# Performance work log

Measured on AMD Instinct MI355X. Metric: run time of the kernel, lower is better.

The kernel has to match this reference:

```python
import jax, jax.numpy as jnp
import numpy as np

DY, DO, DI = 16, 256, 256
BS = 4096
EPS = 1e-6


def setup_inputs() -> dict:
    key = jax.random.key(0)
    k1, k2, k3, k4, k5 = jax.random.split(key, 5)
    k = 1.0 / float(np.sqrt(DY * DI))
    return {
        "x": jax.random.normal(k1, (DY * DI, BS), dtype=jnp.float32),
        "rms_params": jnp.ones((DY * DI,), dtype=jnp.float32)
        + 0.01 * jax.random.normal(k2, (DY * DI,), dtype=jnp.float32),
        "w_upper": jax.random.uniform(k3, (DY, DO, DI), minval=-k, maxval=k, dtype=jnp.float32),
        "w_lower": jax.random.uniform(k4, (DY, DO, DI), minval=-k, maxval=k, dtype=jnp.float32),
        "bias": jax.random.uniform(k5, (DY * DO,), minval=-k, maxval=k, dtype=jnp.float32),
    }


def reference(x, rms_params, w_upper, w_lower, bias):
    # x: (dy*di, bs) features-first layout, matching the torch op.
    dy, do, di = w_upper.shape
    bs = x.shape[1]
    # Per-column RMS factor (fc in the original op is shape (bs,)).
    fc = jax.lax.rsqrt(jnp.mean(x * x, axis=0) + EPS)  # (bs,)
    xn = x * rms_params[:, None] * fc[None, :]          # fused norm+scale
    xb = xn.reshape(dy, di, bs)
    # Dyadic structured matmul: upper acts on block d, lower on its paired
    # (reversed) block dy-1-d.
    up = jnp.einsum("doi,dib->dob", w_upper, xb)
    lo = jnp.einsum("doi,dib->dob", w_lower, xb[::-1])
    y = jax.nn.relu(up + lo + bias.reshape(dy, do, 1))
    return y.reshape(dy * do, bs)
```

## Files before the change

### kernel.cpp

```cpp
#include <hip/hip_runtime.h>

#define DYN 16
#define DON 256
#define DIN 256
#define BSN 4096
#define NF 4096
#define KTOT 512

typedef unsigned short u16;
typedef __attribute__((ext_vector_type(8))) short bf16x8;
typedef __attribute__((ext_vector_type(4))) float f32x4;
typedef __attribute__((ext_vector_type(4))) unsigned short u16x4;

static __device__ __forceinline__ u16 f2bf(float f) {
  unsigned u = __builtin_bit_cast(unsigned, f);
  u += 0x7fffu + ((u >> 16) & 1u);
  return (u16)(u >> 16);
}
static __device__ __forceinline__ float bf2f(u16 h) {
  unsigned u = ((unsigned)h) << 16;
  return __builtin_bit_cast(float, u);
}

__global__ __launch_bounds__(256) void k_pre(
    const float* __restrict__ x, const float* __restrict__ wu,
    const float* __restrict__ wl, const float* __restrict__ rms,
    u16* __restrict__ aprep, u16* __restrict__ xbf,
    float* __restrict__ partial) {
  __shared__ u16 tile[128 * 132];
  const int t = threadIdx.x;
  if (blockIdx.x < 1024) {
    int e = blockIdx.x * 256 + t;
    int row = e >> 6;
    int k0 = (e & 63) << 3;
    int d = row >> 8;
    const float* src;
    const float* rp;
    if (k0 < 256) {
      src = wu + (size_t)row * 256 + k0;
      rp  = rms + d * 256 + k0;
    } else {
      src = wl + (size_t)row * 256 + (k0 - 256);
      rp  = rms + (DYN - 1 - d) * 256 + (k0 - 256);
    }
    float4 s0 = *reinterpret_cast<const float4*>(src);
    float4 s1 = *reinterpret_cast<const float4*>(src + 4);
    float4 r0 = *reinterpret_cast<const float4*>(rp);
    float4 r1 = *reinterpret_cast<const float4*>(rp + 4);
    bf16x8 o;
    o[0] = (short)f2bf(s0.x * r0.x); o[1] = (short)f2bf(s0.y * r0.y);
    o[2] = (short)f2bf(s0.z * r0.z); o[3] = (short)f2bf(s0.w * r0.w);
    o[4] = (short)f2bf(s1.x * r1.x); o[5] = (short)f2bf(s1.y * r1.y);
    o[6] = (short)f2bf(s1.z * r1.z); o[7] = (short)f2bf(s1.w * r1.w);
    *reinterpret_cast<bf16x8*>(aprep + (size_t)row * KTOT + k0) = o;
    return;
  }
  const int bid = blockIdx.x - 1024;
  const int bt = bid & 31, ft = bid >> 5;
  const float* xb = x + (size_t)ft * 128 * BSN + bt * 128;
  const int frow = t >> 5, b4 = (t & 31) * 4;
  #pragma unroll
  for (int p = 0; p < 16; ++p) {
    int f = p * 8 + frow;
    float4 v = *reinterpret_cast<const float4*>(xb + (size_t)f * BSN + b4);
    u16x4 h;
    h[0] = f2bf(v.x); h[1] = f2bf(v.y); h[2] = f2bf(v.z); h[3] = f2bf(v.w);
    *reinterpret_cast<u16x4*>(&tile[f * 132 + b4]) = h;
  }
  __syncthreads();
  const int chunk = t & 15;
  const int bg = t >> 4;
  #pragma unroll
  for (int p = 0; p < 8; ++p) {
    int b = bg + p * 16;
    float s = 0.f;
    bf16x8 w;
    #pragma unroll
    for (int jj = 0; jj < 8; ++jj) {
      int j = (jj + chunk) & 7;
      u16 v = tile[(chunk * 8 + j) * 132 + b];
      float xv = bf2f(v);
      s += xv * xv;
      w[j] = (short)v;
    }
    *reinterpret_cast<bf16x8*>(
        xbf + (size_t)(bt * 128 + b) * NF + ft * 128 + chunk * 8) = w;
    #pragma unroll
    for (int m = 1; m < 16; m <<= 1) s += __shfl_xor(s, m, 64);
    if (chunk == 0) partial[ft * BSN + bt * 128 + b] = s;
  }
}

__global__ __launch_bounds__(512, 4) void k_gemm(
    const u16* __restrict__ aprep, const u16* __restrict__ xbf,
    const float* __restrict__ partial, const float* __restrict__ bias,
    float* __restrict__ out) {
  extern __shared__ char smem[];
  float* fcl = (float*)(smem + 73728);
  const int bid = blockIdx.x;
  const int dp = bid & 7;
  const int s = bid >> 3;
  const int d = (s & 1) ? (15 - dp) : dp;
  const int fh = (s >> 1) & 1;
  const int bt = s >> 2;
  const int b0 = bt * 256;
  const int fr0 = d * 256 + fh * 128;
  const int t = threadIdx.x;
  const int wave = t >> 6, lane = t & 63;
  const int lhi = lane >> 4, llo = lane & 15;
  const int wm = wave >> 2, wn = wave & 3;
  const int kmask = ((llo >> 1) & 7) << 4;

  auto stage = [&](int slot, int kt) {
    const int fbase = (kt < 8) ? (d * 256 + kt * 32)
                               : ((15 - d) * 256 + (kt - 8) * 32);
    #pragma unroll
    for (int j = 0; j < 2; ++j) {
      int c = j * 512 + t;
      int cl = c ^ ((c >> 3) & 7);
      int r = cl >> 2, kc = cl & 3;
      const u16* g = xbf + (size_t)(b0 + r) * NF + fbase + kc * 8;
      unsigned lbase = (unsigned)(slot * 24576 + (j * 512 + wave * 64) * 16);
      __builtin_amdgcn_global_load_lds(
          (const __attribute__((address_space(1))) unsigned int*)g,
          (__attribute__((address_space(3))) unsigned int*)(smem + lbase),
          16, 0, 0);
    }
    {
      int c = t;
      int cl = c ^ ((c >> 3) & 7);
      int r = cl >> 2, kc = cl & 3;
      const u16* g = aprep + (size_t)(fr0 + r) * KTOT + kt * 32 + kc * 8;
      unsigned lbase = (unsigned)(slot * 24576 + 16384 + (wave * 64) * 16);
      __builtin_amdgcn_global_load_lds(
          (const __attribute__((address_space(1))) unsigned int*)g,
          (__attribute__((address_space(3))) unsigned int*)(smem + lbase),
          16, 0, 0);
    }
  };

  if (t < 256) {
    float fs = 0.f;
    #pragma unroll
    for (int i = 0; i < 32; ++i) fs += partial[i * BSN + b0 + t];
    fcl[t] = rsqrtf(fs * (1.0f / 4096.0f) + 1e-6f);
  }

  f32x4 acc[8][2];
  #pragma unroll
  for (int m = 0; m < 8; ++m)
    #pragma unroll
    for (int n = 0; n < 2; ++n)
      acc[m][n] = f32x4{0.f, 0.f, 0.f, 0.f};

  stage(0, 0);
  stage(1, 1);
  asm volatile("s_waitcnt vmcnt(3)\n\ts_barrier" ::: "memory");

  for (int kt = 0; kt < 16; ++kt) {
    const int slot = kt % 3;
    const char* sA = (const char*)smem + slot * 24576;
    const char* sB = sA + 16384;
    if (kt < 14) stage((kt + 2) % 3, kt + 2);

    bf16x8 bq[2], af[4];
    #pragma unroll
    for (int n = 0; n < 2; ++n) {
      int row = wn * 32 + n * 16 + llo;
      bq[n] = *reinterpret_cast<const bf16x8*>(
          sB + ((row * 64 + lhi * 16) ^ kmask));
    }
    #pragma unroll
    for (int m = 0; m < 4; ++m) {
      int row = wm * 128 + m * 16 + llo;
      af[m] = *reinterpret_cast<const bf16x8*>(
          sA + ((row * 64 + lhi * 16) ^ kmask));
    }
    __builtin_amdgcn_s_setprio(1);
    #pragma unroll
    for (int m = 0; m < 4; ++m)
      #pragma unroll
      for (int n = 0; n < 2; ++n)
        acc[m][n] = __builtin_amdgcn_mfma_f32_16x16x32_bf16(
            af[m], bq[n], acc[m][n], 0, 0, 0);
    __builtin_amdgcn_s_setprio(0);
    #pragma unroll
    for (int m = 0; m < 4; ++m) {
      int row = wm * 128 + 64 + m * 16 + llo;
      af[m] = *reinterpret_cast<const bf16x8*>(
          sA + ((row * 64 + lhi * 16) ^ kmask));
    }
    __builtin_amdgcn_s_setprio(1);
    #pragma unroll
    for (int m = 0; m < 4; ++m)
      #pragma unroll
      for (int n = 0; n < 2; ++n)
        acc[4 + m][n] = __builtin_amdgcn_mfma_f32_16x16x32_bf16(
            af[m], bq[n], acc[4 + m][n], 0, 0, 0);
    __builtin_amdgcn_s_setprio(0);

    if (kt < 14) {
      asm volatile("s_waitcnt vmcnt(3)\n\ts_barrier" ::: "memory");
    } else if (kt == 14) {
      asm volatile("s_waitcnt vmcnt(0)\n\ts_barrier" ::: "memory");
    }
  }

  #pragma unroll
  for (int m = 0; m < 8; ++m) {
    int lb = wm * 128 + m * 16 + lhi * 4;
    float4 fq = *reinterpret_cast<const float4*>(&fcl[lb]);
    #pragma unroll
    for (int n = 0; n < 2; ++n) {
      int fo = fr0 + wn * 32 + n * 16 + llo;
      float bv = bias[fo];
      float4 v;
      v.x = fmaxf(acc[m][n][0] * fq.x + bv, 0.f);
      v.y = fmaxf(acc[m][n][1] * fq.y + bv, 0.f);
      v.z = fmaxf(acc[m][n][2] * fq.z + bv, 0.f);
      v.w = fmaxf(acc[m][n][3] * fq.w + bv, 0.f);
      *reinterpret_cast<float4*>(out + (size_t)fo * BSN + b0 + lb) = v;
    }
  }
}

extern "C" void kernel_launch(void* const* d_in, const int* in_sizes, int n_in,
                              void* d_out, int out_size, void* d_ws, size_t ws_size,
                              hipStream_t stream) {
  (void)in_sizes; (void)n_in; (void)out_size; (void)ws_size;
  const float* x    = (const float*)d_in[0];
  const float* rms  = (const float*)d_in[1];
  const float* wu   = (const float*)d_in[2];
  const float* wl   = (const float*)d_in[3];
  const float* bias = (const float*)d_in[4];
  float* out = (float*)d_out;

  char* ws = (char*)d_ws;
  u16* xbf      = (u16*)ws;
  u16* aprep    = (u16*)(ws + 33554432);
  float* partial = (float*)(ws + 37748736);

  k_pre<<<2048, 256, 0, stream>>>(x, wu, wl, rms, aprep, xbf, partial);
  k_gemm<<<512, 512, 74752, stream>>>(aprep, xbf, partial, bias, out);
}
```

Measured before the change: 57.51 us.

## Retile GEMM to 128x256 blocks with 4 waves and swizzle pre-pass LDS tile

The GEMM block tile changes from 256 batch x 128 features with 8 waves to 128 batch x 256 features with 4 waves. Each wave now holds a 64x128 accumulator tile, which gives more MFMA work per LDS fragment load, and the weight tile is staged in four async loads instead of one. Separately, the pre-pass LDS transpose tile uses an XOR swizzle on the column index in place of the rotated read order, to cut bank conflicts. Risks are higher register pressure from 128 accumulator floats per thread and fewer waves per block, which reduces the ability to hide latency.

```diff
diff --git a/kernel.cpp b/kernel.cpp
--- a/kernel.cpp
+++ b/kernel.cpp
@@ -65,7 +65,7 @@
     float4 v = *reinterpret_cast<const float4*>(xb + (size_t)f * BSN + b4);
     u16x4 h;
     h[0] = f2bf(v.x); h[1] = f2bf(v.y); h[2] = f2bf(v.z); h[3] = f2bf(v.w);
-    *reinterpret_cast<u16x4*>(&tile[f * 132 + b4]) = h;
+    *reinterpret_cast<u16x4*>(&tile[f * 132 + (b4 ^ ((f >> 3) << 2))]) = h;
   }
   __syncthreads();
   const int chunk = t & 15;
@@ -76,9 +76,9 @@
     float s = 0.f;
     bf16x8 w;
     #pragma unroll
-    for (int jj = 0; jj < 8; ++jj) {
-      int j = (jj + chunk) & 7;
-      u16 v = tile[(chunk * 8 + j) * 132 + b];
+    for (int j = 0; j < 8; ++j) {
+      int r = chunk * 8 + j;
+      u16 v = tile[r * 132 + (b ^ ((r >> 3) << 2))];
       float xv = bf2f(v);
       s += xv * xv;
       w[j] = (short)v;
@@ -91,7 +91,7 @@
   }
 }
 
-__global__ __launch_bounds__(512, 4) void k_gemm(
+__global__ __launch_bounds__(256, 2) void k_gemm(
     const u16* __restrict__ aprep, const u16* __restrict__ xbf,
     const float* __restrict__ partial, const float* __restrict__ bias,
     float* __restrict__ out) {
@@ -101,37 +101,45 @@
   const int dp = bid & 7;
   const int s = bid >> 3;
   const int d = (s & 1) ? (15 - dp) : dp;
-  const int fh = (s >> 1) & 1;
-  const int bt = s >> 2;
-  const int b0 = bt * 256;
-  const int fr0 = d * 256 + fh * 128;
+  const int bt = s >> 1;
+  const int b0 = bt * 128;
+  const int fr0 = d * 256;
   const int t = threadIdx.x;
   const int wave = t >> 6, lane = t & 63;
   const int lhi = lane >> 4, llo = lane & 15;
-  const int wm = wave >> 2, wn = wave & 3;
+  const int wm = wave >> 1, wn = wave & 1;
   const int kmask = ((llo >> 1) & 7) << 4;
+
+  f32x4 acc[4][8];
+  #pragma unroll
+  for (int m = 0; m < 4; ++m)
+    #pragma unroll
+    for (int n = 0; n < 8; ++n)
+      acc[m][n] = f32x4{0.f, 0.f, 0.f, 0.f};
 
   auto stage = [&](int slot, int kt) {
     const int fbase = (kt < 8) ? (d * 256 + kt * 32)
                                : ((15 - d) * 256 + (kt - 8) * 32);
     #pragma unroll
     for (int j = 0; j < 2; ++j) {
-      int c = j * 512 + t;
+      int c = j * 256 + t;
       int cl = c ^ ((c >> 3) & 7);
       int r = cl >> 2, kc = cl & 3;
       const u16* g = xbf + (size_t)(b0 + r) * NF + fbase + kc * 8;
-      unsigned lbase = (unsigned)(slot * 24576 + (j * 512 + wave * 64) * 16);
+      unsigned lbase = (unsigned)(slot * 24576 + (j * 256 + wave * 64) * 16);
       __builtin_amdgcn_global_load_lds(
           (const __attribute__((address_space(1))) unsigned int*)g,
           (__attribute__((address_space(3))) unsigned int*)(smem + lbase),
           16, 0, 0);
     }
-    {
-      int c = t;
+    #pragma unroll
+    for (int j = 0; j < 4; ++j) {
+      int c = j * 256 + t;
       int cl = c ^ ((c >> 3) & 7);
       int r = cl >> 2, kc = cl & 3;
       const u16* g = aprep + (size_t)(fr0 + r) * KTOT + kt * 32 + kc * 8;
-      unsigned lbase = (unsigned)(slot * 24576 + 16384 + (wave * 64) * 16);
+      unsigned lbase = (unsigned)(slot * 24576 + 8192 +
+                                  (j * 256 + wave * 64) * 16);
       __builtin_amdgcn_global_load_lds(
           (const __attribute__((address_space(1))) unsigned int*)g,
           (__attribute__((address_space(3))) unsigned int*)(smem + lbase),
@@ -139,80 +147,58 @@
     }
   };
 
-  if (t < 256) {
+  if (t < 128) {
     float fs = 0.f;
     #pragma unroll
     for (int i = 0; i < 32; ++i) fs += partial[i * BSN + b0 + t];
     fcl[t] = rsqrtf(fs * (1.0f / 4096.0f) + 1e-6f);
   }
-
-  f32x4 acc[8][2];
-  #pragma unroll
-  for (int m = 0; m < 8; ++m)
-    #pragma unroll
-    for (int n = 0; n < 2; ++n)
-      acc[m][n] = f32x4{0.f, 0.f, 0.f, 0.f};
-
   stage(0, 0);
   stage(1, 1);
-  asm volatile("s_waitcnt vmcnt(3)\n\ts_barrier" ::: "memory");
+  asm volatile("s_waitcnt vmcnt(6)\n\ts_barrier" ::: "memory");
 
   for (int kt = 0; kt < 16; ++kt) {
     const int slot = kt % 3;
     const char* sA = (const char*)smem + slot * 24576;
-    const char* sB = sA + 16384;
+    const char* sB = sA + 8192;
     if (kt < 14) stage((kt + 2) % 3, kt + 2);
 
-    bf16x8 bq[2], af[4];
-    #pragma unroll
-    for (int n = 0; n < 2; ++n) {
-      int row = wn * 32 + n * 16 + llo;
+    bf16x8 af[4], bq[8];
+    #pragma unroll
+    for (int m = 0; m < 4; ++m) {
+      int row = wm * 64 + m * 16 + llo;
+      af[m] = *reinterpret_cast<const bf16x8*>(
+          sA + ((row * 64 + lhi * 16) ^ kmask));
+    }
+    #pragma unroll
+    for (int n = 0; n < 8; ++n) {
+      int row = wn * 128 + n * 16 + llo;
       bq[n] = *reinterpret_cast<const bf16x8*>(
           sB + ((row * 64 + lhi * 16) ^ kmask));
     }
-    #pragma unroll
-    for (int m = 0; m < 4; ++m) {
-      int row = wm * 128 + m * 16 + llo;
-      af[m] = *reinterpret_cast<const bf16x8*>(
-          sA + ((row * 64 + lhi * 16) ^ kmask));
-    }
     __builtin_amdgcn_s_setprio(1);
     #pragma unroll
     for (int m = 0; m < 4; ++m)
       #pragma unroll
-      for (int n = 0; n < 2; ++n)
+      for (int n = 0; n < 8; ++n)
         acc[m][n] = __builtin_amdgcn_mfma_f32_16x16x32_bf16(
             af[m], bq[n], acc[m][n], 0, 0, 0);
     __builtin_amdgcn_s_setprio(0);
-    #pragma unroll
-    for (int m = 0; m < 4; ++m) {
-      int row = wm * 128 + 64 + m * 16 + llo;
-      af[m] = *reinterpret_cast<const bf16x8*>(
-          sA + ((row * 64 + lhi * 16) ^ kmask));
-    }
-    __builtin_amdgcn_s_setprio(1);
-    #pragma unroll
-    for (int m = 0; m < 4; ++m)
-      #pragma unroll
-      for (int n = 0; n < 2; ++n)
-        acc[4 + m][n] = __builtin_amdgcn_mfma_f32_16x16x32_bf16(
-            af[m], bq[n], acc[4 + m][n], 0, 0, 0);
-    __builtin_amdgcn_s_setprio(0);
 
     if (kt < 14) {
-      asm volatile("s_waitcnt vmcnt(3)\n\ts_barrier" ::: "memory");
+      asm volatile("s_waitcnt vmcnt(6)\n\ts_barrier" ::: "memory");
     } else if (kt == 14) {
       asm volatile("s_waitcnt vmcnt(0)\n\ts_barrier" ::: "memory");
     }
   }
 
   #pragma unroll
-  for (int m = 0; m < 8; ++m) {
-    int lb = wm * 128 + m * 16 + lhi * 4;
+  for (int m = 0; m < 4; ++m) {
+    int lb = wm * 64 + m * 16 + lhi * 4;
     float4 fq = *reinterpret_cast<const float4*>(&fcl[lb]);
     #pragma unroll
-    for (int n = 0; n < 2; ++n) {
-      int fo = fr0 + wn * 32 + n * 16 + llo;
+    for (int n = 0; n < 8; ++n) {
+      int fo = fr0 + wn * 128 + n * 16 + llo;
       float bv = bias[fo];
       float4 v;
       v.x = fmaxf(acc[m][n][0] * fq.x + bv, 0.f);
@@ -241,5 +227,5 @@
   float* partial = (float*)(ws + 37748736);
 
   k_pre<<<2048, 256, 0, stream>>>(x, wu, wl, rms, aprep, xbf, partial);
-  k_gemm<<<512, 512, 74752, stream>>>(aprep, xbf, partial, bias, out);
-}
+  k_gemm<<<512, 256, 74240, stream>>>(aprep, xbf, partial, bias, out);
+}
```

New measurement: 53.39 us. 1.08x faster.
